# Kernel tuning notes

Measured on AMD Instinct MI355X. Metric: run time of the kernel, lower is better.

## Reference

```python
import jax, jax.numpy as jnp
import numpy as np

N = 8192      # num nodes = feature dim (A is NxN adjacency used as features)
H = 1024      # bottleneck dim
E = 8192      # num edges
PENALTY = 10.0  # scalar buffer from __init__


def setup_inputs() -> dict:
    key = jax.random.key(0)
    ks = jax.random.split(key, 7)
    return {
        "A": jax.random.normal(ks[0], (N, N), dtype=jnp.float32),
        "W1": jax.random.normal(ks[1], (H, N), dtype=jnp.float32) * 0.02,
        "b1": jax.random.normal(ks[2], (H,), dtype=jnp.float32) * 0.02,
        "W2": jax.random.normal(ks[3], (N, H), dtype=jnp.float32) * 0.02,
        "b2": jax.random.normal(ks[4], (N,), dtype=jnp.float32) * 0.02,
        "edges": jax.random.randint(ks[5], (E, 2), 0, N, dtype=jnp.int32),
        "labels": jax.random.randint(ks[6], (E,), 0, 2, dtype=jnp.int32),
    }


def reference(A, W1, b1, W2, b2, edges, labels):
    ni = edges[:, 0]
    nj = edges[:, 1]
    Xi = A[ni]  # [E, N]
    Xj = A[nj]  # [E, N]
    lab = labels.astype(A.dtype)

    layers = [(W1, b1), (W2, b2)]
    Hi, Hj = Xi, Xj
    loss_1 = jnp.zeros((), A.dtype)
    loss_r_per_edge = jnp.zeros((), A.dtype)
    for (W, b) in layers:
        Hi = jax.nn.sigmoid(Hi @ W.T + b)
        Hj = jax.nn.sigmoid(Hj @ W.T + b)
        # per-edge L2 norm of activation diff at this layer, weighted by label
        loss_1 = loss_1 + jnp.sum(jnp.linalg.norm(Hi - Hj, axis=1) * lab)
        # original code appends weight-row-norm sum + bias norm once per (edge, layer)
        loss_r_per_edge = loss_r_per_edge + jnp.sum(jnp.linalg.norm(W, axis=1)) + jnp.linalg.norm(b)
    loss_r = loss_r_per_edge * jnp.asarray(E, A.dtype)

    # reconstruction loss; penalty scales the diff when label >= 1 (scalar => factors out of norm)
    factor = jnp.where(lab >= 1.0, jnp.asarray(PENALTY, A.dtype), jnp.asarray(1.0, A.dtype))
    loss_2 = jnp.sum(factor * (jnp.linalg.norm(Xi - Hi, axis=1) + jnp.linalg.norm(Xj - Hj, axis=1)))

    return loss_1 + loss_2 + loss_r
```

## Files before the change

### kernel.cpp

```cpp
#include <hip/hip_runtime.h>
#include <hip/hip_bf16.h>
#include <stdint.h>

#define N_DIM 8192
#define H_DIM 1024
#define E_DIM 8192
#define PENALTY_F 10.0f
#define WSCALE 16.0f
#define INV_WSCALE 0.0625f

typedef unsigned short u16;
typedef unsigned char u8;
typedef unsigned int u32;
typedef __attribute__((ext_vector_type(4))) float f32x4;
typedef __attribute__((ext_vector_type(2))) float f32x2;
typedef __attribute__((ext_vector_type(4))) int i32x4;
typedef __attribute__((ext_vector_type(8))) int i32x8;

__device__ __forceinline__ u32 pack4_fp8(float a, float b, float c, float d) {
  u32 p = __builtin_amdgcn_cvt_pk_fp8_f32(a, b, 0, false);
  p = __builtin_amdgcn_cvt_pk_fp8_f32(c, d, p, true);
  return p;
}
__device__ __forceinline__ f32x2 unpk_lo(u32 v) {
  return __builtin_amdgcn_cvt_pk_f32_fp8(v, false);
}
__device__ __forceinline__ f32x2 unpk_hi(u32 v) {
  return __builtin_amdgcn_cvt_pk_f32_fp8(v, true);
}

#define GLD16(ldsptr, gptr)                                                     \
  __builtin_amdgcn_global_load_lds(                                             \
      (__attribute__((address_space(1))) void*)(gptr),                          \
      (__attribute__((address_space(3))) void*)(ldsptr), 16, 0, 0)

__device__ __forceinline__ float wave_red(float v) {
  for (int o = 32; o; o >>= 1) v += __shfl_down(v, o, 64);
  return v;
}

__device__ __forceinline__ float block_reduce1(float v) {
  __shared__ float buf[4];
  v = wave_red(v);
  int lane = threadIdx.x & 63, w = threadIdx.x >> 6;
  if (lane == 0) buf[w] = v;
  __syncthreads();
  float r = 0.f;
  if (threadIdx.x == 0) r = buf[0] + buf[1] + buf[2] + buf[3];
  return r;
}

__global__ void convert_f32_fp8(const float* __restrict__ in,
                                u8* __restrict__ out, int n4, float scale) {
  int i = blockIdx.x * blockDim.x + threadIdx.x;
  if (i < n4) {
    float4 v = ((const float4*)in)[i];
    ((u32*)out)[i] =
        pack4_fp8(v.x * scale, v.y * scale, v.z * scale, v.w * scale);
  }
}

__global__ void prep_w(const float* __restrict__ W1,
                       const float* __restrict__ W2,
                       const float* __restrict__ b1,
                       const float* __restrict__ b2, u8* __restrict__ W1_8,
                       u8* __restrict__ W2_8, float* __restrict__ out) {
  const int blk = blockIdx.x;
  if (blk < H_DIM) {
    const float4* row = (const float4*)(W1 + (size_t)blk * N_DIM);
    u32* orow = (u32*)(W1_8 + (size_t)blk * N_DIM);
    float s = 0.f;
#pragma unroll
    for (int t = 0; t < 8; ++t) {
      int i = threadIdx.x + t * 256;
      float4 v = row[i];
      s += v.x * v.x + v.y * v.y + v.z * v.z + v.w * v.w;
      orow[i] = pack4_fp8(v.x * WSCALE, v.y * WSCALE, v.z * WSCALE,
                          v.w * WSCALE);
    }
    s = block_reduce1(s);
    if (threadIdx.x == 0) atomicAdd(out, sqrtf(s) * (float)E_DIM);
  } else if (blk < H_DIM + N_DIM / 4) {
    __shared__ float buf[4];
    const int wave = threadIdx.x >> 6, lane = threadIdx.x & 63;
    const int r = (blk - H_DIM) * 4 + wave;
    const float4* row = (const float4*)(W2 + (size_t)r * H_DIM);
    u32* orow = (u32*)(W2_8 + (size_t)r * H_DIM);
    float s = 0.f;
#pragma unroll
    for (int t = 0; t < 4; ++t) {
      int i = lane + t * 64;
      float4 v = row[i];
      s += v.x * v.x + v.y * v.y + v.z * v.z + v.w * v.w;
      orow[i] = pack4_fp8(v.x * WSCALE, v.y * WSCALE, v.z * WSCALE,
                          v.w * WSCALE);
    }
    s = wave_red(s);
    if (lane == 0) buf[wave] = sqrtf(s);
    __syncthreads();
    if (threadIdx.x == 0)
      atomicAdd(out, (buf[0] + buf[1] + buf[2] + buf[3]) * (float)E_DIM);
  } else if (blk == H_DIM + N_DIM / 4) {
    const float4* row = (const float4*)b1;
    float4 v = row[threadIdx.x];
    float s = v.x * v.x + v.y * v.y + v.z * v.z + v.w * v.w;
    s = block_reduce1(s);
    if (threadIdx.x == 0) atomicAdd(out, sqrtf(s) * (float)E_DIM);
  } else {
    const float4* row = (const float4*)b2;
    float s = 0.f;
#pragma unroll
    for (int t = 0; t < 8; ++t) {
      float4 v = row[threadIdx.x + t * 256];
      s += v.x * v.x + v.y * v.y + v.z * v.z + v.w * v.w;
    }
    s = block_reduce1(s);
    if (threadIdx.x == 0) atomicAdd(out, sqrtf(s) * (float)E_DIM);
  }
}

#define BM 128
#define BN 128
#define BKB 128

__global__ __launch_bounds__(256) void gemm_fp8_sigmoid(
    const u8* __restrict__ Ag,
    const u8* __restrict__ Bg,
    const float* __restrict__ bias,
    u8* __restrict__ Cg,
    float invScale, int K, int Nd) {
  __shared__ __align__(16) u8 Xs[BM * BKB];
  __shared__ __align__(16) u8 Ws[BN * BKB];

  const int nwg = gridDim.x * gridDim.y;
  const int id = blockIdx.y * gridDim.x + blockIdx.x;
  const int wg = (id & 7) * (nwg >> 3) + (id >> 3);
  const int bx = wg % gridDim.x;
  const int by = wg / gridDim.x;

  const int tid = threadIdx.x;
  const int wave = tid >> 6, lane = tid & 63;
  const int wr = wave >> 1, wc = wave & 1;
  const size_t rowBase = (size_t)by * BM;
  const size_t colBase = (size_t)bx * BN;

  f32x4 acc[4][4] = {};

  const int i8 = lane >> 3;
  const int c8 = lane & 7;
  const int sw = c8 ^ i8;

  const int quad = lane >> 4;
  const int m15 = lane & 15;

  for (int k0 = 0; k0 < K; k0 += BKB) {
#pragma unroll
    for (int j = 0; j < 4; ++j) {
      const int r0 = (wave * 4 + j) * 8;
      const u8* gx = Ag + (rowBase + r0 + i8) * (size_t)K + (k0 + sw * 16);
      GLD16(&Xs[r0 * BKB], gx);
      const u8* gw = Bg + (colBase + r0 + i8) * (size_t)K + (k0 + sw * 16);
      GLD16(&Ws[r0 * BKB], gw);
    }
    __syncthreads();

    i32x8 af[4], bfr[4];
#pragma unroll
    for (int t = 0; t < 4; ++t) {
      const int m = wr * 64 + t * 16 + m15;
      i32x4 alo = *(const i32x4*)&Xs[m * BKB + ((2 * quad) ^ (m & 7)) * 16];
      i32x4 ahi = *(const i32x4*)&Xs[m * BKB + ((2 * quad + 1) ^ (m & 7)) * 16];
      af[t] = __builtin_shufflevector(alo, ahi, 0, 1, 2, 3, 4, 5, 6, 7);
      const int n = wc * 64 + t * 16 + m15;
      i32x4 blo = *(const i32x4*)&Ws[n * BKB + ((2 * quad) ^ (n & 7)) * 16];
      i32x4 bhi = *(const i32x4*)&Ws[n * BKB + ((2 * quad + 1) ^ (n & 7)) * 16];
      bfr[t] = __builtin_shufflevector(blo, bhi, 0, 1, 2, 3, 4, 5, 6, 7);
    }
#pragma unroll
    for (int mt = 0; mt < 4; ++mt)
#pragma unroll
      for (int nt = 0; nt < 4; ++nt)
        acc[mt][nt] = __builtin_amdgcn_mfma_scale_f32_16x16x128_f8f6f4(
            bfr[nt], af[mt], acc[mt][nt], 0, 0,
            0, 0x7F7F7F7F, 0, 0x7F7F7F7F);
    __syncthreads();
  }

  f32x4 bv4[4];
#pragma unroll
  for (int nt = 0; nt < 4; ++nt)
    bv4[nt] = *(const f32x4*)&bias[colBase + wc * 64 + nt * 16 + quad * 4];
#pragma unroll
  for (int mt = 0; mt < 4; ++mt) {
    const size_t grow = rowBase + wr * 64 + mt * 16 + m15;
    u32* crow = (u32*)(Cg + grow * (size_t)Nd + colBase + wc * 64);
#pragma unroll
    for (int nt = 0; nt < 4; ++nt) {
      float v[4];
#pragma unroll
      for (int i = 0; i < 4; ++i) {
        float x = acc[mt][nt][i] * invScale + bv4[nt][i];
        v[i] = WSCALE / (1.0f + __expf(-x));
      }
      crow[nt * 4 + quad] = pack4_fp8(v[0], v[1], v[2], v[3]);
    }
  }
}

#define BM2 256
#define BN2 256

__global__ __launch_bounds__(512, 2) void gemm2_fp8_sigmoid(
    const u8* __restrict__ Ag,
    const u8* __restrict__ Bg,
    const float* __restrict__ bias,
    u8* __restrict__ Cg,
    float invScale, int K, int Nd) {
  __shared__ __align__(16) u8 Xs[2][BM2 * BKB];
  __shared__ __align__(16) u8 Ws[2][BN2 * BKB];

  const int tid = threadIdx.x;
  const int wave = tid >> 6, lane = tid & 63;
  const int wr = wave >> 2;
  const int wc = wave & 3;
  const size_t rowBase = (size_t)blockIdx.y * BM2;
  const size_t colBase = (size_t)blockIdx.x * BN2;

  f32x4 acc[8][4] = {};

  const int i8 = lane >> 3;
  const int c8 = lane & 7;
  const int sw = c8 ^ i8;
  const int quad = lane >> 4;
  const int m15 = lane & 15;

  const int T = K / BKB;

  auto STAGE = [&](int kt, int b) {
    const size_t kOff = (size_t)kt * BKB + sw * 16;
#pragma unroll
    for (int j = 0; j < 4; ++j) {
      const int r0 = (wave * 4 + j) * 8;
      GLD16(&Xs[b][r0 * BKB], Ag + (rowBase + r0 + i8) * (size_t)K + kOff);
      GLD16(&Ws[b][r0 * BKB], Bg + (colBase + r0 + i8) * (size_t)K + kOff);
    }
  };

  STAGE(0, 0);
  __syncthreads();

  for (int t = 0; t < T; ++t) {
    const int cur = t & 1;
    if (t + 1 < T) STAGE(t + 1, cur ^ 1);

    const u8* Xb = Xs[cur];
    const u8* Wb = Ws[cur];

    i32x8 bfr[4];
#pragma unroll
    for (int nt = 0; nt < 4; ++nt) {
      const int n = wc * 64 + nt * 16 + m15;
      i32x4 blo = *(const i32x4*)&Wb[n * BKB + ((2 * quad) ^ (n & 7)) * 16];
      i32x4 bhi = *(const i32x4*)&Wb[n * BKB + ((2 * quad + 1) ^ (n & 7)) * 16];
      bfr[nt] = __builtin_shufflevector(blo, bhi, 0, 1, 2, 3, 4, 5, 6, 7);
    }
#pragma unroll
    for (int mt = 0; mt < 8; ++mt) {
      const int m = wr * 128 + mt * 16 + m15;
      i32x4 alo = *(const i32x4*)&Xb[m * BKB + ((2 * quad) ^ (m & 7)) * 16];
      i32x4 ahi = *(const i32x4*)&Xb[m * BKB + ((2 * quad + 1) ^ (m & 7)) * 16];
      i32x8 af = __builtin_shufflevector(alo, ahi, 0, 1, 2, 3, 4, 5, 6, 7);
#pragma unroll
      for (int nt = 0; nt < 4; ++nt)
        acc[mt][nt] = __builtin_amdgcn_mfma_scale_f32_16x16x128_f8f6f4(
            bfr[nt], af, acc[mt][nt], 0, 0,
            0, 0x7F7F7F7F, 0, 0x7F7F7F7F);
    }
    __syncthreads();
  }

  f32x4 bv4[4];
#pragma unroll
  for (int nt = 0; nt < 4; ++nt)
    bv4[nt] = *(const f32x4*)&bias[colBase + wc * 64 + nt * 16 + quad * 4];
#pragma unroll
  for (int mt = 0; mt < 8; ++mt) {
    const size_t grow = rowBase + wr * 128 + mt * 16 + m15;
    u32* crow = (u32*)(Cg + grow * (size_t)Nd + colBase + wc * 64);
#pragma unroll
    for (int nt = 0; nt < 4; ++nt) {
      float v[4];
#pragma unroll
      for (int i = 0; i < 4; ++i) {
        float x = acc[mt][nt][i] * invScale + bv4[nt][i];
        v[i] = WSCALE / (1.0f + __expf(-x));
      }
      crow[nt * 4 + quad] = pack4_fp8(v[0], v[1], v[2], v[3]);
    }
  }
}

__global__ void edge_loss_h(const u8* __restrict__ H1,
                            const int* __restrict__ edges,
                            const int* __restrict__ labels,
                            float* __restrict__ out) {
  __shared__ float buf[4];
  const int wave = threadIdx.x >> 6, lane = threadIdx.x & 63;
  const int e = blockIdx.x * 4 + wave;
  float r = 0.f;
  if (labels[e] != 0) {
    const int ni = edges[e * 2], nj = edges[e * 2 + 1];
    const i32x4 a = ((const i32x4*)(H1 + (size_t)ni * H_DIM))[lane];
    const i32x4 b = ((const i32x4*)(H1 + (size_t)nj * H_DIM))[lane];
    float s = 0.f;
#pragma unroll
    for (int j = 0; j < 4; ++j) {
      f32x2 al = unpk_lo((u32)a[j]), ah = unpk_hi((u32)a[j]);
      f32x2 bl = unpk_lo((u32)b[j]), bh = unpk_hi((u32)b[j]);
      float d0 = al.x - bl.x, d1 = al.y - bl.y;
      float d2 = ah.x - bh.x, d3 = ah.y - bh.y;
      s += d0 * d0 + d1 * d1 + d2 * d2 + d3 * d3;
    }
    s = wave_red(s);
    r = sqrtf(s) * INV_WSCALE;
  }
  if (lane == 0) buf[wave] = r;
  __syncthreads();
  if (threadIdx.x == 0) atomicAdd(out, buf[0] + buf[1] + buf[2] + buf[3]);
}

__global__ void edge_loss_final(const u8* __restrict__ H2,
                                const u8* __restrict__ A8,
                                const int* __restrict__ edges,
                                const int* __restrict__ labels,
                                float* __restrict__ out) {
  __shared__ float buf[4];
  const int wave = threadIdx.x >> 6, lane = threadIdx.x & 63;
  const int e = blockIdx.x * 4 + wave;
  const int ni = edges[e * 2], nj = edges[e * 2 + 1];
  const i32x4* hi = (const i32x4*)(H2 + (size_t)ni * N_DIM);
  const i32x4* hj = (const i32x4*)(H2 + (size_t)nj * N_DIM);
  const i32x4* xi = (const i32x4*)(A8 + (size_t)ni * N_DIM);
  const i32x4* xj = (const i32x4*)(A8 + (size_t)nj * N_DIM);
  float s12 = 0.f, si = 0.f, sj = 0.f;
#pragma unroll 2
  for (int t = 0; t < 8; ++t) {
    const int idx = lane + t * 64;
    i32x4 a = hi[idx], b = hj[idx], x = xi[idx], y = xj[idx];
#pragma unroll
    for (int j = 0; j < 4; ++j) {
      f32x2 al = unpk_lo((u32)a[j]), ah = unpk_hi((u32)a[j]);
      f32x2 bl = unpk_lo((u32)b[j]), bh = unpk_hi((u32)b[j]);
      f32x2 xl = unpk_lo((u32)x[j]), xh = unpk_hi((u32)x[j]);
      f32x2 yl = unpk_lo((u32)y[j]), yh = unpk_hi((u32)y[j]);
      float d;
      d = al.x - bl.x; s12 += d * d;
      d = al.y - bl.y; s12 += d * d;
      d = ah.x - bh.x; s12 += d * d;
      d = ah.y - bh.y; s12 += d * d;
      d = WSCALE * xl.x - al.x; si += d * d;
      d = WSCALE * xl.y - al.y; si += d * d;
      d = WSCALE * xh.x - ah.x; si += d * d;
      d = WSCALE * xh.y - ah.y; si += d * d;
      d = WSCALE * yl.x - bl.x; sj += d * d;
      d = WSCALE * yl.y - bl.y; sj += d * d;
      d = WSCALE * yh.x - bh.x; sj += d * d;
      d = WSCALE * yh.y - bh.y; sj += d * d;
    }
  }
  for (int o = 32; o; o >>= 1) {
    s12 += __shfl_down(s12, o, 64);
    si += __shfl_down(si, o, 64);
    sj += __shfl_down(sj, o, 64);
  }
  if (lane == 0) {
    float lab = (labels[e] != 0) ? 1.f : 0.f;
    float fac = (labels[e] != 0) ? PENALTY_F : 1.f;
    buf[wave] = (lab * sqrtf(s12) + fac * (sqrtf(si) + sqrtf(sj))) * INV_WSCALE;
  }
  __syncthreads();
  if (threadIdx.x == 0) atomicAdd(out, buf[0] + buf[1] + buf[2] + buf[3]);
}

extern "C" void kernel_launch(void* const* d_in, const int* in_sizes, int n_in,
                              void* d_out, int out_size, void* d_ws,
                              size_t ws_size, hipStream_t stream) {
  const float* A = (const float*)d_in[0];
  const float* W1 = (const float*)d_in[1];
  const float* b1 = (const float*)d_in[2];
  const float* W2 = (const float*)d_in[3];
  const float* b2 = (const float*)d_in[4];
  const int* edges = (const int*)d_in[5];
  const int* labels = (const int*)d_in[6];
  float* out = (float*)d_out;

  char* ws = (char*)d_ws;
  u8* A8   = (u8*)(ws);
  u8* H1_8 = (u8*)(ws + 67108864ull);
  u8* H2_8 = (u8*)(ws + 75497472ull);
  u8* W1_8 = (u8*)(ws + 142606336ull);
  u8* W2_8 = (u8*)(ws + 150994944ull);

  hipMemsetAsync(out, 0, sizeof(float), stream);

  convert_f32_fp8<<<(N_DIM * N_DIM / 4 + 255) / 256, 256, 0, stream>>>(
      A, A8, N_DIM * N_DIM / 4, 1.0f);

  prep_w<<<H_DIM + N_DIM / 4 + 2, 256, 0, stream>>>(W1, W2, b1, b2, W1_8,
                                                    W2_8, out);

  gemm_fp8_sigmoid<<<dim3(H_DIM / BN, N_DIM / BM), 256, 0, stream>>>(
      A8, W1_8, b1, H1_8, INV_WSCALE, N_DIM, H_DIM);
  edge_loss_h<<<E_DIM / 4, 256, 0, stream>>>(H1_8, edges, labels, out);

  gemm2_fp8_sigmoid<<<dim3(N_DIM / BN2, N_DIM / BM2), 512, 0, stream>>>(
      H1_8, W2_8, b2, H2_8, INV_WSCALE * INV_WSCALE, H_DIM, N_DIM);
  edge_loss_final<<<E_DIM / 4, 256, 0, stream>>>(H2_8, A8, edges, labels, out);
}
```

Measured before the change: 704.4 us.

## Compute only rows of nodes referenced by edges via compaction

Marks the nodes that appear in the edge list, builds a compact permutation with a single-block scan, and converts and gathers only those rows of A to fp8. Both GEMMs exit early for row tiles beyond the compacted count, and the edge-loss kernels index through a slot map. With 8192 random edges over 8192 nodes, about 86% of nodes are referenced, so the saving is partial. The change adds small marking and scan kernels, and it also raises wave priority around the MFMA loop in the second GEMM.

```diff
diff --git a/kernel.cpp b/kernel.cpp
--- a/kernel.cpp
+++ b/kernel.cpp
@@ -50,13 +50,62 @@
   return r;
 }
 
-__global__ void convert_f32_fp8(const float* __restrict__ in,
-                                u8* __restrict__ out, int n4, float scale) {
-  int i = blockIdx.x * blockDim.x + threadIdx.x;
-  if (i < n4) {
-    float4 v = ((const float4*)in)[i];
-    ((u32*)out)[i] =
-        pack4_fp8(v.x * scale, v.y * scale, v.z * scale, v.w * scale);
+__global__ void mark_nodes(const int* __restrict__ edges,
+                           int* __restrict__ mark) {
+  int t = blockIdx.x * blockDim.x + threadIdx.x;
+  if (t < 2 * E_DIM) mark[edges[t]] = 1;
+}
+
+__global__ void scan_nodes(const int* __restrict__ mark, int* __restrict__ perm,
+                           int* __restrict__ slot, int* __restrict__ countP) {
+  const int t = threadIdx.x;
+  const int base = t * 32;
+  u32 bits = 0;
+#pragma unroll
+  for (int k = 0; k < 32; ++k) bits |= (mark[base + k] ? 1u : 0u) << k;
+  int local = __popc(bits);
+  const int lane = t & 63, w = t >> 6;
+  int pre = local;
+  for (int o = 1; o < 64; o <<= 1) {
+    int g = __shfl_up(pre, o, 64);
+    if (lane >= o) pre += g;
+  }
+  __shared__ int wsum[4];
+  __shared__ int tot;
+  if (lane == 63) wsum[w] = pre;
+  __syncthreads();
+  int wbase = 0;
+  for (int i = 0; i < w; ++i) wbase += wsum[i];
+  const int excl = wbase + pre - local;
+  int run = excl;
+#pragma unroll
+  for (int k = 0; k < 32; ++k)
+    if (bits & (1u << k)) {
+      slot[base + k] = run;
+      perm[run] = base + k;
+      run++;
+    }
+  if (t == 255) tot = excl + local;
+  __syncthreads();
+  const int count = tot;
+  const int cpad = (count + 255) & ~255;
+  for (int r = count + t; r < cpad; r += 256) perm[r] = 0;
+  if (t == 0) countP[0] = cpad;
+}
+
+__global__ void convert_gather(const float* __restrict__ A,
+                               u8* __restrict__ A8c,
+                               const int* __restrict__ perm,
+                               const int* __restrict__ countP) {
+  const int r = blockIdx.x;
+  if (r >= countP[0]) return;
+  const float4* row = (const float4*)(A + (size_t)perm[r] * N_DIM);
+  u32* orow = (u32*)(A8c + (size_t)r * N_DIM);
+#pragma unroll
+  for (int t = 0; t < 8; ++t) {
+    const int i = threadIdx.x + t * 256;
+    float4 v = row[i];
+    orow[i] = pack4_fp8(v.x, v.y, v.z, v.w);
   }
 }
 
@@ -128,7 +177,7 @@
     const u8* __restrict__ Bg,
     const float* __restrict__ bias,
     u8* __restrict__ Cg,
-    float invScale, int K, int Nd) {
+    float invScale, int K, int Nd, const int* __restrict__ countP) {
   __shared__ __align__(16) u8 Xs[BM * BKB];
   __shared__ __align__(16) u8 Ws[BN * BKB];
 
@@ -137,6 +186,9 @@
   const int wg = (id & 7) * (nwg >> 3) + (id >> 3);
   const int bx = wg % gridDim.x;
   const int by = wg / gridDim.x;
+
+  const int Mp = countP[0];
+  if (by * BM >= Mp) return;
 
   const int tid = threadIdx.x;
   const int wave = tid >> 6, lane = tid & 63;
@@ -215,9 +267,12 @@
     const u8* __restrict__ Bg,
     const float* __restrict__ bias,
     u8* __restrict__ Cg,
-    float invScale, int K, int Nd) {
+    float invScale, int K, int Nd, const int* __restrict__ countP) {
   __shared__ __align__(16) u8 Xs[2][BM2 * BKB];
   __shared__ __align__(16) u8 Ws[2][BN2 * BKB];
+
+  const int Mp = countP[0];
+  if ((int)blockIdx.y * BM2 >= Mp) return;
 
   const int tid = threadIdx.x;
   const int wave = tid >> 6, lane = tid & 63;
@@ -264,6 +319,7 @@
       i32x4 bhi = *(const i32x4*)&Wb[n * BKB + ((2 * quad + 1) ^ (n & 7)) * 16];
       bfr[nt] = __builtin_shufflevector(blo, bhi, 0, 1, 2, 3, 4, 5, 6, 7);
     }
+    __builtin_amdgcn_s_setprio(1);
 #pragma unroll
     for (int mt = 0; mt < 8; ++mt) {
       const int m = wr * 128 + mt * 16 + m15;
@@ -276,6 +332,7 @@
             bfr[nt], af, acc[mt][nt], 0, 0,
             0, 0x7F7F7F7F, 0, 0x7F7F7F7F);
     }
+    __builtin_amdgcn_s_setprio(0);
     __syncthreads();
   }
 
@@ -303,13 +360,14 @@
 __global__ void edge_loss_h(const u8* __restrict__ H1,
                             const int* __restrict__ edges,
                             const int* __restrict__ labels,
+                            const int* __restrict__ slot,
                             float* __restrict__ out) {
   __shared__ float buf[4];
   const int wave = threadIdx.x >> 6, lane = threadIdx.x & 63;
   const int e = blockIdx.x * 4 + wave;
   float r = 0.f;
   if (labels[e] != 0) {
-    const int ni = edges[e * 2], nj = edges[e * 2 + 1];
+    const int ni = slot[edges[e * 2]], nj = slot[edges[e * 2 + 1]];
     const i32x4 a = ((const i32x4*)(H1 + (size_t)ni * H_DIM))[lane];
     const i32x4 b = ((const i32x4*)(H1 + (size_t)nj * H_DIM))[lane];
     float s = 0.f;
@@ -333,11 +391,12 @@
                                 const u8* __restrict__ A8,
                                 const int* __restrict__ edges,
                                 const int* __restrict__ labels,
+                                const int* __restrict__ slot,
                                 float* __restrict__ out) {
   __shared__ float buf[4];
   const int wave = threadIdx.x >> 6, lane = threadIdx.x & 63;
   const int e = blockIdx.x * 4 + wave;
-  const int ni = edges[e * 2], nj = edges[e * 2 + 1];
+  const int ni = slot[edges[e * 2]], nj = slot[edges[e * 2 + 1]];
   const i32x4* hi = (const i32x4*)(H2 + (size_t)ni * N_DIM);
   const i32x4* hj = (const i32x4*)(H2 + (size_t)nj * N_DIM);
   const i32x4* xi = (const i32x4*)(A8 + (size_t)ni * N_DIM);
@@ -395,25 +454,33 @@
   float* out = (float*)d_out;
 
   char* ws = (char*)d_ws;
-  u8* A8   = (u8*)(ws);
-  u8* H1_8 = (u8*)(ws + 67108864ull);
-  u8* H2_8 = (u8*)(ws + 75497472ull);
+  u8* A8c  = (u8*)(ws);
+  u8* H1c  = (u8*)(ws + 67108864ull);
+  u8* H2c  = (u8*)(ws + 75497472ull);
   u8* W1_8 = (u8*)(ws + 142606336ull);
   u8* W2_8 = (u8*)(ws + 150994944ull);
+  int* mark   = (int*)(ws + 159383552ull);
+  int* perm   = (int*)(ws + 159416320ull);
+  int* slot   = (int*)(ws + 159449088ull);
+  int* countP = (int*)(ws + 159481856ull);
 
   hipMemsetAsync(out, 0, sizeof(float), stream);
-
-  convert_f32_fp8<<<(N_DIM * N_DIM / 4 + 255) / 256, 256, 0, stream>>>(
-      A, A8, N_DIM * N_DIM / 4, 1.0f);
+  hipMemsetAsync(mark, 0, N_DIM * sizeof(int), stream);
+
+  mark_nodes<<<(2 * E_DIM) / 256, 256, 0, stream>>>(edges, mark);
+  scan_nodes<<<1, 256, 0, stream>>>(mark, perm, slot, countP);
+
+  convert_gather<<<N_DIM, 256, 0, stream>>>(A, A8c, perm, countP);
 
   prep_w<<<H_DIM + N_DIM / 4 + 2, 256, 0, stream>>>(W1, W2, b1, b2, W1_8,
                                                     W2_8, out);
 
   gemm_fp8_sigmoid<<<dim3(H_DIM / BN, N_DIM / BM), 256, 0, stream>>>(
-      A8, W1_8, b1, H1_8, INV_WSCALE, N_DIM, H_DIM);
-  edge_loss_h<<<E_DIM / 4, 256, 0, stream>>>(H1_8, edges, labels, out);
+      A8c, W1_8, b1, H1c, INV_WSCALE, N_DIM, H_DIM, countP);
+  edge_loss_h<<<E_DIM / 4, 256, 0, stream>>>(H1c, edges, labels, slot, out);
 
   gemm2_fp8_sigmoid<<<dim3(N_DIM / BN2, N_DIM / BM2), 512, 0, stream>>>(
-      H1_8, W2_8, b2, H2_8, INV_WSCALE * INV_WSCALE, H_DIM, N_DIM);
-  edge_loss_final<<<E_DIM / 4, 256, 0, stream>>>(H2_8, A8, edges, labels, out);
-}
+      H1c, W2_8, b2, H2c, INV_WSCALE * INV_WSCALE, H_DIM, N_DIM, countP);
+  edge_loss_final<<<E_DIM / 4, 256, 0, stream>>>(H2c, A8c, edges, labels, slot,
+                                                 out);
+}
```

Result: slower. 728.1 us (+3.4%).

## Fuse per-node reconstruction norms into GEMM2 epilogue and shard loss atomics

Applied to the files above, without the earlier changes.

The squared reconstruction distance ||X - H2|| for each node row is now computed in the GEMM2 epilogue, which reads the A8 tile alongside the freshly packed output and accumulates per-row sums through LDS atomics into a global nd2 buffer. edge_loss_final then only gathers H2 rows for the pair-difference term and looks up nd2, so it no longer re-gathers two A8 rows per edge. Scalar loss atomics are spread over 64 padded partial slots and summed by a small finalize kernel, which cuts contention on a single address. The A conversion becomes a grid-stride loop with a fixed grid, and s_setprio is raised around the MFMA loop. The epilogue gains an extra A8 read of all N×N entries plus atomics, and per-node norms are computed for every node rather than only those touched by edges.

```diff
diff --git a/kernel.cpp b/kernel.cpp
--- a/kernel.cpp
+++ b/kernel.cpp
@@ -34,6 +34,8 @@
       (__attribute__((address_space(1))) void*)(gptr),                          \
       (__attribute__((address_space(3))) void*)(ldsptr), 16, 0, 0)
 
+#define PSLOT(part) (&(part)[(blockIdx.x & 63) * 16])
+
 __device__ __forceinline__ float wave_red(float v) {
   for (int o = 32; o; o >>= 1) v += __shfl_down(v, o, 64);
   return v;
@@ -52,8 +54,8 @@
 
 __global__ void convert_f32_fp8(const float* __restrict__ in,
                                 u8* __restrict__ out, int n4, float scale) {
-  int i = blockIdx.x * blockDim.x + threadIdx.x;
-  if (i < n4) {
+  const int stride = gridDim.x * blockDim.x;
+  for (int i = blockIdx.x * blockDim.x + threadIdx.x; i < n4; i += stride) {
     float4 v = ((const float4*)in)[i];
     ((u32*)out)[i] =
         pack4_fp8(v.x * scale, v.y * scale, v.z * scale, v.w * scale);
@@ -64,8 +66,9 @@
                        const float* __restrict__ W2,
                        const float* __restrict__ b1,
                        const float* __restrict__ b2, u8* __restrict__ W1_8,
-                       u8* __restrict__ W2_8, float* __restrict__ out) {
+                       u8* __restrict__ W2_8, float* __restrict__ part) {
   const int blk = blockIdx.x;
+  float* slotp = PSLOT(part);
   if (blk < H_DIM) {
     const float4* row = (const float4*)(W1 + (size_t)blk * N_DIM);
     u32* orow = (u32*)(W1_8 + (size_t)blk * N_DIM);
@@ -79,7 +82,7 @@
                           v.w * WSCALE);
     }
     s = block_reduce1(s);
-    if (threadIdx.x == 0) atomicAdd(out, sqrtf(s) * (float)E_DIM);
+    if (threadIdx.x == 0) atomicAdd(slotp, sqrtf(s) * (float)E_DIM);
   } else if (blk < H_DIM + N_DIM / 4) {
     __shared__ float buf[4];
     const int wave = threadIdx.x >> 6, lane = threadIdx.x & 63;
@@ -99,13 +102,13 @@
     if (lane == 0) buf[wave] = sqrtf(s);
     __syncthreads();
     if (threadIdx.x == 0)
-      atomicAdd(out, (buf[0] + buf[1] + buf[2] + buf[3]) * (float)E_DIM);
+      atomicAdd(slotp, (buf[0] + buf[1] + buf[2] + buf[3]) * (float)E_DIM);
   } else if (blk == H_DIM + N_DIM / 4) {
     const float4* row = (const float4*)b1;
     float4 v = row[threadIdx.x];
     float s = v.x * v.x + v.y * v.y + v.z * v.z + v.w * v.w;
     s = block_reduce1(s);
-    if (threadIdx.x == 0) atomicAdd(out, sqrtf(s) * (float)E_DIM);
+    if (threadIdx.x == 0) atomicAdd(slotp, sqrtf(s) * (float)E_DIM);
   } else {
     const float4* row = (const float4*)b2;
     float s = 0.f;
@@ -115,7 +118,7 @@
       s += v.x * v.x + v.y * v.y + v.z * v.z + v.w * v.w;
     }
     s = block_reduce1(s);
-    if (threadIdx.x == 0) atomicAdd(out, sqrtf(s) * (float)E_DIM);
+    if (threadIdx.x == 0) atomicAdd(slotp, sqrtf(s) * (float)E_DIM);
   }
 }
 
@@ -215,6 +218,8 @@
     const u8* __restrict__ Bg,
     const float* __restrict__ bias,
     u8* __restrict__ Cg,
+    const u8* __restrict__ A8,
+    float* __restrict__ nd2,
     float invScale, int K, int Nd) {
   __shared__ __align__(16) u8 Xs[2][BM2 * BKB];
   __shared__ __align__(16) u8 Ws[2][BN2 * BKB];
@@ -264,6 +269,7 @@
       i32x4 bhi = *(const i32x4*)&Wb[n * BKB + ((2 * quad + 1) ^ (n & 7)) * 16];
       bfr[nt] = __builtin_shufflevector(blo, bhi, 0, 1, 2, 3, 4, 5, 6, 7);
     }
+    __builtin_amdgcn_s_setprio(1);
 #pragma unroll
     for (int mt = 0; mt < 8; ++mt) {
       const int m = wr * 128 + mt * 16 + m15;
@@ -276,8 +282,13 @@
             bfr[nt], af, acc[mt][nt], 0, 0,
             0, 0x7F7F7F7F, 0, 0x7F7F7F7F);
     }
+    __builtin_amdgcn_s_setprio(0);
     __syncthreads();
   }
+
+  float* ndbuf = (float*)&Xs[0][0];
+  if (tid < 256) ndbuf[tid] = 0.f;
+  __syncthreads();
 
   f32x4 bv4[4];
 #pragma unroll
@@ -285,8 +296,11 @@
     bv4[nt] = *(const f32x4*)&bias[colBase + wc * 64 + nt * 16 + quad * 4];
 #pragma unroll
   for (int mt = 0; mt < 8; ++mt) {
-    const size_t grow = rowBase + wr * 128 + mt * 16 + m15;
+    const int rowLocal = wr * 128 + mt * 16 + m15;
+    const size_t grow = rowBase + rowLocal;
     u32* crow = (u32*)(Cg + grow * (size_t)Nd + colBase + wc * 64);
+    const u32* arow = (const u32*)(A8 + grow * (size_t)Nd + colBase + wc * 64);
+    float nds = 0.f;
 #pragma unroll
     for (int nt = 0; nt < 4; ++nt) {
       float v[4];
@@ -295,15 +309,27 @@
         float x = acc[mt][nt][i] * invScale + bv4[nt][i];
         v[i] = WSCALE / (1.0f + __expf(-x));
       }
-      crow[nt * 4 + quad] = pack4_fp8(v[0], v[1], v[2], v[3]);
-    }
-  }
+      const u32 packed = pack4_fp8(v[0], v[1], v[2], v[3]);
+      crow[nt * 4 + quad] = packed;
+      f32x2 hlo = unpk_lo(packed), hhi = unpk_hi(packed);
+      const u32 xa = arow[nt * 4 + quad];
+      f32x2 xlo = unpk_lo(xa), xhi = unpk_hi(xa);
+      float d;
+      d = WSCALE * xlo.x - hlo.x; nds += d * d;
+      d = WSCALE * xlo.y - hlo.y; nds += d * d;
+      d = WSCALE * xhi.x - hhi.x; nds += d * d;
+      d = WSCALE * xhi.y - hhi.y; nds += d * d;
+    }
+    atomicAdd(&ndbuf[rowLocal], nds);
+  }
+  __syncthreads();
+  if (tid < 256) atomicAdd(&nd2[rowBase + tid], ndbuf[tid]);
 }
 
 __global__ void edge_loss_h(const u8* __restrict__ H1,
                             const int* __restrict__ edges,
                             const int* __restrict__ labels,
-                            float* __restrict__ out) {
+                            float* __restrict__ part) {
   __shared__ float buf[4];
   const int wave = threadIdx.x >> 6, lane = threadIdx.x & 63;
   const int e = blockIdx.x * 4 + wave;
@@ -326,60 +352,54 @@
   }
   if (lane == 0) buf[wave] = r;
   __syncthreads();
-  if (threadIdx.x == 0) atomicAdd(out, buf[0] + buf[1] + buf[2] + buf[3]);
+  if (threadIdx.x == 0)
+    atomicAdd(PSLOT(part), buf[0] + buf[1] + buf[2] + buf[3]);
 }
 
 __global__ void edge_loss_final(const u8* __restrict__ H2,
-                                const u8* __restrict__ A8,
+                                const float* __restrict__ nd2,
                                 const int* __restrict__ edges,
                                 const int* __restrict__ labels,
-                                float* __restrict__ out) {
+                                float* __restrict__ part) {
   __shared__ float buf[4];
   const int wave = threadIdx.x >> 6, lane = threadIdx.x & 63;
   const int e = blockIdx.x * 4 + wave;
   const int ni = edges[e * 2], nj = edges[e * 2 + 1];
   const i32x4* hi = (const i32x4*)(H2 + (size_t)ni * N_DIM);
   const i32x4* hj = (const i32x4*)(H2 + (size_t)nj * N_DIM);
-  const i32x4* xi = (const i32x4*)(A8 + (size_t)ni * N_DIM);
-  const i32x4* xj = (const i32x4*)(A8 + (size_t)nj * N_DIM);
-  float s12 = 0.f, si = 0.f, sj = 0.f;
+  float s12 = 0.f;
 #pragma unroll 2
   for (int t = 0; t < 8; ++t) {
     const int idx = lane + t * 64;
-    i32x4 a = hi[idx], b = hj[idx], x = xi[idx], y = xj[idx];
+    i32x4 a = hi[idx], b = hj[idx];
 #pragma unroll
     for (int j = 0; j < 4; ++j) {
       f32x2 al = unpk_lo((u32)a[j]), ah = unpk_hi((u32)a[j]);
       f32x2 bl = unpk_lo((u32)b[j]), bh = unpk_hi((u32)b[j]);
-      f32x2 xl = unpk_lo((u32)x[j]), xh = unpk_hi((u32)x[j]);
-      f32x2 yl = unpk_lo((u32)y[j]), yh = unpk_hi((u32)y[j]);
       float d;
       d = al.x - bl.x; s12 += d * d;
       d = al.y - bl.y; s12 += d * d;
       d = ah.x - bh.x; s12 += d * d;
       d = ah.y - bh.y; s12 += d * d;
-      d = WSCALE * xl.x - al.x; si += d * d;
-      d = WSCALE * xl.y - al.y; si += d * d;
-      d = WSCALE * xh.x - ah.x; si += d * d;
-      d = WSCALE * xh.y - ah.y; si += d * d;
-      d = WSCALE * yl.x - bl.x; sj += d * d;
-      d = WSCALE * yl.y - bl.y; sj += d * d;
-      d = WSCALE * yh.x - bh.x; sj += d * d;
-      d = WSCALE * yh.y - bh.y; sj += d * d;
-    }
-  }
-  for (int o = 32; o; o >>= 1) {
-    s12 += __shfl_down(s12, o, 64);
-    si += __shfl_down(si, o, 64);
-    sj += __shfl_down(sj, o, 64);
-  }
+    }
+  }
+  s12 = wave_red(s12);
   if (lane == 0) {
     float lab = (labels[e] != 0) ? 1.f : 0.f;
     float fac = (labels[e] != 0) ? PENALTY_F : 1.f;
-    buf[wave] = (lab * sqrtf(s12) + fac * (sqrtf(si) + sqrtf(sj))) * INV_WSCALE;
-  }
-  __syncthreads();
-  if (threadIdx.x == 0) atomicAdd(out, buf[0] + buf[1] + buf[2] + buf[3]);
+    buf[wave] = (lab * sqrtf(s12) + fac * (sqrtf(nd2[ni]) + sqrtf(nd2[nj]))) *
+                INV_WSCALE;
+  }
+  __syncthreads();
+  if (threadIdx.x == 0)
+    atomicAdd(PSLOT(part), buf[0] + buf[1] + buf[2] + buf[3]);
+}
+
+__global__ void finalize_sum(const float* __restrict__ part,
+                             float* __restrict__ out) {
+  float v = part[threadIdx.x * 16];
+  v = wave_red(v);
+  if (threadIdx.x == 0) atomicAdd(out, v);
 }
 
 extern "C" void kernel_launch(void* const* d_in, const int* in_sizes, int n_in,
@@ -400,20 +420,26 @@
   u8* H2_8 = (u8*)(ws + 75497472ull);
   u8* W1_8 = (u8*)(ws + 142606336ull);
   u8* W2_8 = (u8*)(ws + 150994944ull);
+  float* nd2  = (float*)(ws + 159383552ull);
+  float* part = (float*)(ws + 159416320ull);
 
   hipMemsetAsync(out, 0, sizeof(float), stream);
-
-  convert_f32_fp8<<<(N_DIM * N_DIM / 4 + 255) / 256, 256, 0, stream>>>(
-      A, A8, N_DIM * N_DIM / 4, 1.0f);
+  hipMemsetAsync(nd2, 0, N_DIM * sizeof(float) + 64 * 16 * sizeof(float),
+                 stream);
+
+  convert_f32_fp8<<<2048, 256, 0, stream>>>(A, A8, N_DIM * N_DIM / 4, 1.0f);
 
   prep_w<<<H_DIM + N_DIM / 4 + 2, 256, 0, stream>>>(W1, W2, b1, b2, W1_8,
-                                                    W2_8, out);
+                                                    W2_8, part);
 
   gemm_fp8_sigmoid<<<dim3(H_DIM / BN, N_DIM / BM), 256, 0, stream>>>(
       A8, W1_8, b1, H1_8, INV_WSCALE, N_DIM, H_DIM);
-  edge_loss_h<<<E_DIM / 4, 256, 0, stream>>>(H1_8, edges, labels, out);
+  edge_loss_h<<<E_DIM / 4, 256, 0, stream>>>(H1_8, edges, labels, part);
 
   gemm2_fp8_sigmoid<<<dim3(N_DIM / BN2, N_DIM / BM2), 512, 0, stream>>>(
-      H1_8, W2_8, b2, H2_8, INV_WSCALE * INV_WSCALE, H_DIM, N_DIM);
-  edge_loss_final<<<E_DIM / 4, 256, 0, stream>>>(H2_8, A8, edges, labels, out);
-}
+      H1_8, W2_8, b2, H2_8, A8, nd2, INV_WSCALE * INV_WSCALE, H_DIM, N_DIM);
+  edge_loss_final<<<E_DIM / 4, 256, 0, stream>>>(H2_8, nd2, edges, labels,
+                                                 part);
+
+  finalize_sum<<<1, 64, 0, stream>>>(part, out);
+}
```

Measured after the change: 653.8 us. -7.2%, faster.
